# Kernel tuning notes

Measured on AMD Instinct MI355X. Metric: run time of the kernel, lower is better.

Reference implementation:

```python
import jax, jax.numpy as jnp
import numpy as np

L2_REG = 0.02


def setup_inputs() -> dict:
    key = jax.random.key(0)
    k1, k2 = jax.random.split(key)
    n, d = 4096, 1024
    anchors = jax.random.normal(k1, (n, d), dtype=jnp.float32)
    positives = jax.random.normal(k2, (n, d), dtype=jnp.float32)
    return {"anchors": anchors, "positives": positives}


def reference(anchors, positives):
    # Fused equivalent of the per-row masked_select loop:
    # x[i, j] = a_i . (p_j - p_i) = S[i, j] - S[i, i], for j != i
    n = anchors.shape[0]
    S = anchors @ positives.T                     # (n, n)
    x = S - jnp.diag(S)[:, None]                  # subtract anchor-positive sim per row
    offdiag = ~jnp.eye(n, dtype=bool)
    # sum over negatives j != i of exp(x[i, j])
    s = jnp.sum(jnp.where(offdiag, jnp.exp(x), 0.0), axis=1)  # (n,)
    n_pair = jnp.mean(jnp.log1p(s))
    l2 = jnp.sum(anchors ** 2 + positives ** 2) / n
    return n_pair + L2_REG * l2
```

## Files before the change

### kernel.cpp

```cpp
#include <hip/hip_runtime.h>
#include <math.h>
#include <stdint.h>

#define N 4096
#define Dm 1024
#define BK 64
#define NT (Dm / BK)
#define NCB (N / 64)
#define NPART 512

typedef __attribute__((ext_vector_type(8))) short bf16x8;
typedef __attribute__((ext_vector_type(4))) float f32x4;

typedef const void __attribute__((address_space(1)))* gas_t;
typedef void __attribute__((address_space(3)))* las_t;

static __device__ __forceinline__ void gload_lds16(const void* g, void* l) {
    __builtin_amdgcn_global_load_lds((gas_t)g, (las_t)l, 16, 0, 0);
}

static __device__ __forceinline__ unsigned short f2bf(float f) {
    unsigned int u = __float_as_uint(f);
    unsigned int r = (u + 0x7fff + ((u >> 16) & 1)) >> 16;
    return (unsigned short)r;
}

__global__ __launch_bounds__(256) void prep_kernel(const float* __restrict__ A,
                                                   const float* __restrict__ P,
                                                   unsigned short* __restrict__ Abf,
                                                   unsigned short* __restrict__ Pbf,
                                                   float* __restrict__ D,
                                                   float* __restrict__ rowl2) {
    int t = threadIdx.x;
    int lane = t & 63;
    int row = blockIdx.x * 4 + (t >> 6);
    const float4* a4 = (const float4*)(A + (size_t)row * Dm);
    const float4* p4 = (const float4*)(P + (size_t)row * Dm);
    ushort4* ao = (ushort4*)(Abf + (size_t)row * Dm);
    ushort4* po = (ushort4*)(Pbf + (size_t)row * Dm);
    float dot = 0.0f, l2 = 0.0f;
#pragma unroll
    for (int c = 0; c < 4; ++c) {
        int idx = c * 64 + lane;
        float4 a = a4[idx], p = p4[idx];
        ushort4 ab, pb;
        ab.x = f2bf(a.x); ab.y = f2bf(a.y); ab.z = f2bf(a.z); ab.w = f2bf(a.w);
        pb.x = f2bf(p.x); pb.y = f2bf(p.y); pb.z = f2bf(p.z); pb.w = f2bf(p.w);
        ao[idx] = ab; po[idx] = pb;
        dot += a.x * p.x + a.y * p.y + a.z * p.z + a.w * p.w;
        l2  += a.x * a.x + a.y * a.y + a.z * a.z + a.w * a.w
             + p.x * p.x + p.y * p.y + p.z * p.z + p.w * p.w;
    }
#pragma unroll
    for (int off = 32; off; off >>= 1) {
        dot += __shfl_xor(dot, off, 64);
        l2  += __shfl_xor(l2,  off, 64);
    }
    if (lane == 0) {
        D[row]     = dot;
        rowl2[row] = l2;
    }
}

#define STAGE_TILE(gp, lp, kt) do {                                            \
        gload_lds16((gp) + (kt),                    (lp)         + tid * 8);   \
        gload_lds16((gp) + (kt) +  64 * (size_t)Dm, (lp) + 4096  + tid * 8);   \
        gload_lds16((gp) + (kt) + 128 * (size_t)Dm, (lp) + 8192  + tid * 8);   \
        gload_lds16((gp) + (kt) + 192 * (size_t)Dm, (lp) + 12288 + tid * 8);   \
    } while (0)

#define STAGE_B_HALF(lpB, kt, h) do {                                          \
        gload_lds16(gB + (kt) + ((h) ? 128 * (size_t)Dm : (size_t)0),          \
                    (lpB) + (h) * 8192 + tid * 8);                             \
        gload_lds16(gB + (kt) + ((h) ? 192 * (size_t)Dm : 64 * (size_t)Dm),    \
                    (lpB) + (h) * 8192 + 4096 + tid * 8);                      \
    } while (0)

#define READ_A4(dst, buf, rg0) do {                                            \
        dst[0] = *(const bf16x8*)((buf) + ((rg0)     * 16) * BK + aoff0);      \
        dst[1] = *(const bf16x8*)((buf) + ((rg0)     * 16) * BK + aoff1);      \
        dst[2] = *(const bf16x8*)((buf) + ((rg0) + 1) * 16 * BK + aoff0);      \
        dst[3] = *(const bf16x8*)((buf) + ((rg0) + 1) * 16 * BK + aoff1);      \
    } while (0)

#define READ_B8(PAR, buf) do {                                                 \
        _Pragma("unroll")                                                      \
        for (int j = 0; j < 4; ++j) {                                          \
            bfr[PAR][j][0] = *(const bf16x8*)((buf) + j * 16 * BK + aoff0);    \
            bfr[PAR][j][1] = *(const bf16x8*)((buf) + j * 16 * BK + aoff1);    \
        }                                                                      \
    } while (0)

#define MFMA_PH(P, ap, BP)                                                     \
    _Pragma("unroll")                                                          \
    for (int j = 0; j < 4; ++j)                                                \
        acc[2*(P)][j]   = __builtin_amdgcn_mfma_f32_16x16x32_bf16(ap[0], bfr[BP][j][0], acc[2*(P)][j],   0, 0, 0); \
    _Pragma("unroll")                                                          \
    for (int j = 0; j < 4; ++j)                                                \
        acc[2*(P)][j]   = __builtin_amdgcn_mfma_f32_16x16x32_bf16(ap[1], bfr[BP][j][1], acc[2*(P)][j],   0, 0, 0); \
    _Pragma("unroll")                                                          \
    for (int j = 0; j < 4; ++j)                                                \
        acc[2*(P)+1][j] = __builtin_amdgcn_mfma_f32_16x16x32_bf16(ap[2], bfr[BP][j][0], acc[2*(P)+1][j], 0, 0, 0); \
    _Pragma("unroll")                                                          \
    for (int j = 0; j < 4; ++j)                                                \
        acc[2*(P)+1][j] = __builtin_amdgcn_mfma_f32_16x16x32_bf16(ap[3], bfr[BP][j][1], acc[2*(P)+1][j], 0, 0, 0);

#define TILE_BODY(CUR, NXT) do {                                               \
        const unsigned short* aT  = aBase + (CUR) * 16384;                     \
        const unsigned short* aTn = aBase + (NXT) * 16384;                     \
        const unsigned short* bTn = bBase + (NXT) * 16384;                     \
        unsigned short* stA = &As[NXT][0];                                     \
        unsigned short* stB = &Bs[CUR][0];                                     \
         \
        READ_A4(aF[1], aT, 2);                                                 \
        if (t >= 1 && t <= 14) STAGE_TILE(gA, stA, (t + 1) * BK);              \
        __builtin_amdgcn_sched_barrier(0);                                     \
        __builtin_amdgcn_s_setprio(1);                                         \
        MFMA_PH(0, aF[0], CUR)                                                 \
        __builtin_amdgcn_s_setprio(0);                                         \
        __builtin_amdgcn_sched_barrier(0);                                     \
        __builtin_amdgcn_s_barrier();                                          \
         \
        READ_A4(aF[0], aT, 4);                                                 \
        if (t <= 13) STAGE_B_HALF(stB, (t + 2) * BK, 0);                       \
        __builtin_amdgcn_sched_barrier(0);                                     \
        __builtin_amdgcn_s_setprio(1);                                         \
        MFMA_PH(1, aF[1], CUR)                                                 \
        __builtin_amdgcn_s_setprio(0);                                         \
        __builtin_amdgcn_sched_barrier(0);                                     \
        __builtin_amdgcn_s_barrier();                                          \
         \
        READ_A4(aF[1], aT, 6);                                                 \
        if (t <= 13) STAGE_B_HALF(stB, (t + 2) * BK, 1);                       \
        __builtin_amdgcn_sched_barrier(0);                                     \
        __builtin_amdgcn_s_setprio(1);                                         \
        MFMA_PH(2, aF[0], CUR)                                                 \
        __builtin_amdgcn_s_setprio(0);                                         \
        __builtin_amdgcn_sched_barrier(0);                                     \
        __builtin_amdgcn_s_barrier();                                          \
           \
        if (t <= 13)      { asm volatile("s_waitcnt vmcnt(4)" ::: "memory"); } \
        else if (t == 14) { asm volatile("s_waitcnt vmcnt(0)" ::: "memory"); } \
        if (t <= 14) {                                                         \
            __builtin_amdgcn_s_barrier();                                      \
            __builtin_amdgcn_sched_barrier(0);                                 \
            READ_B8(NXT, bTn);                                                 \
            READ_A4(aF[0], aTn, 0);                                            \
        }                                                                      \
        __builtin_amdgcn_sched_barrier(0);                                     \
        __builtin_amdgcn_s_setprio(1);                                         \
        MFMA_PH(3, aF[1], CUR)                                                 \
        __builtin_amdgcn_s_setprio(0);                                         \
        __builtin_amdgcn_sched_barrier(0);                                     \
        if (t <= 13) __builtin_amdgcn_s_barrier();                             \
    } while (0)

__global__ __launch_bounds__(512, 2) void npair_mfma(const unsigned short* __restrict__ Abf,
                                                     const unsigned short* __restrict__ Pbf,
                                                     const float* __restrict__ D,
                                                     float* __restrict__ Mpart,
                                                     float* __restrict__ Spart) {
    __shared__ unsigned short As[2][256 * BK];
    __shared__ unsigned short Bs[2][256 * BK];

    int tid = threadIdx.x;
    int lane = tid & 63;
    int wid = tid >> 6;
    int wr = wid >> 2, wc = wid & 3;

    int bid = blockIdx.y * gridDim.x + blockIdx.x;
    int xcd = bid & 7, lid = bid >> 3;
    int by = (xcd >> 1) * 4 + (lid >> 3);
    int bx = (xcd & 1) * 8 + (lid & 7);
    int row0 = by * 256, col0 = bx * 256;

    int srow = tid >> 3;
    int kcol = (tid & 7) ^ (srow & 7);
    const unsigned short* gA = Abf + (size_t)(row0 + srow) * Dm + (kcol << 3);
    const unsigned short* gB = Pbf + (size_t)(col0 + srow) * Dm + (kcol << 3);

    STAGE_TILE(gA, &As[0][0], 0);
    STAGE_TILE(gB, &Bs[0][0], 0);
    STAGE_TILE(gA, &As[1][0], BK);
    STAGE_TILE(gB, &Bs[1][0], BK);
    asm volatile("s_waitcnt vmcnt(8)" ::: "memory");
    __builtin_amdgcn_s_barrier();
    __builtin_amdgcn_sched_barrier(0);

    int l15 = lane & 15;
    int aoff0 = (((lane >> 4)    ) ^ (lane & 7)) << 3;
    int aoff1 = (((lane >> 4) + 4) ^ (lane & 7)) << 3;
    const unsigned short* aBase = &As[0][0] + (wr * 128 + l15) * BK;
    const unsigned short* bBase = &Bs[0][0] + (wc * 64  + l15) * BK;

    f32x4 acc[8][4] = {};
    bf16x8 bfr[2][4][2];
    bf16x8 aF[2][4];

    READ_B8(0, bBase);
    READ_A4(aF[0], aBase, 0);

    for (int tt = 0; tt < NT / 2; ++tt) {
        int t = 2 * tt;
        TILE_BODY(0, 1);
        t = 2 * tt + 1;
        TILE_BODY(1, 0);
    }

    __builtin_amdgcn_sched_barrier(0);

    int cb = bx * 4 + wc;
#pragma unroll
    for (int i = 0; i < 8; ++i) {
        int rloc = wr * 128 + i * 16 + ((lane >> 4) << 2);
#pragma unroll
        for (int e = 0; e < 4; ++e) {
            int gr = row0 + rloc + e;
            float Dv = D[gr];
            float xs[4];
            float m = -INFINITY;
#pragma unroll
            for (int j = 0; j < 4; ++j) {
                int gc = col0 + wc * 64 + j * 16 + (lane & 15);
                float x = acc[i][j][e] - Dv;
                if (gr == gc) x = -INFINITY;
                xs[j] = x;
                m = fmaxf(m, x);
            }
#pragma unroll
            for (int off = 8; off; off >>= 1) m = fmaxf(m, __shfl_xor(m, off, 64));
            float s = 0.0f;
#pragma unroll
            for (int j = 0; j < 4; ++j) s += __expf(xs[j] - m);
#pragma unroll
            for (int off = 8; off; off >>= 1) s += __shfl_xor(s, off, 64);
            if ((lane & 15) == 0) {
                Mpart[(size_t)gr * NCB + cb] = m;
                Spart[(size_t)gr * NCB + cb] = s;
            }
        }
    }
}

__global__ __launch_bounds__(256) void combine_rows(const float* __restrict__ Mpart,
                                                    const float* __restrict__ Spart,
                                                    const float* __restrict__ rowl2,
                                                    float* __restrict__ partL,
                                                    float* __restrict__ partR) {
    int t = threadIdx.x;
    int lane = t & 63;
    int w = t >> 6;
    __shared__ float ls[8];
#pragma unroll
    for (int r = 0; r < 2; ++r) {
        int row = blockIdx.x * 8 + w * 2 + r;
        float mp = Mpart[(size_t)row * NCB + lane];
        float sp = Spart[(size_t)row * NCB + lane];
        float m = mp;
#pragma unroll
        for (int off = 32; off; off >>= 1) m = fmaxf(m, __shfl_xor(m, off, 64));
        float s = sp * __expf(mp - m);
#pragma unroll
        for (int off = 32; off; off >>= 1) s += __shfl_xor(s, off, 64);
        if (lane == 0) ls[w * 2 + r] = m + logf(__expf(-m) + s);
    }
    __syncthreads();
    if (t == 0) {
        int r8 = blockIdx.x * 8;
        float L = 0.0f, R = 0.0f;
#pragma unroll
        for (int r = 0; r < 8; ++r) { L += ls[r]; R += rowl2[r8 + r]; }
        partL[blockIdx.x] = L;
        partR[blockIdx.x] = R;
    }
}

__global__ __launch_bounds__(256) void final_reduce(const float* __restrict__ partL,
                                                    const float* __restrict__ partR,
                                                    float* __restrict__ out) {
    int t = threadIdx.x;
    float accL = partL[t] + partL[t + 256];
    float acc2 = partR[t] + partR[t + 256];
#pragma unroll
    for (int off = 32; off; off >>= 1) {
        accL += __shfl_xor(accL, off, 64);
        acc2 += __shfl_xor(acc2, off, 64);
    }
    __shared__ float sa[4], sb[4];
    int wave = t >> 6;
    if ((t & 63) == 0) { sa[wave] = accL; sb[wave] = acc2; }
    __syncthreads();
    if (t == 0) {
        float L  = sa[0] + sa[1] + sa[2] + sa[3];
        float l2 = sb[0] + sb[1] + sb[2] + sb[3];
        out[0] = L / (float)N + 0.02f * (l2 / (float)N);
    }
}

extern "C" void kernel_launch(void* const* d_in, const int* in_sizes, int n_in,
                              void* d_out, int out_size, void* d_ws, size_t ws_size,
                              hipStream_t stream) {
    const float* A = (const float*)d_in[0];
    const float* P = (const float*)d_in[1];
    float* out = (float*)d_out;

    unsigned short* Abf = (unsigned short*)d_ws;
    unsigned short* Pbf = Abf + (size_t)N * Dm;
    float* D     = (float*)(Pbf + (size_t)N * Dm);
    float* rowl2 = D + N;
    float* partL = rowl2 + N;
    float* partR = partL + NPART;
    float* Mpart = partR + NPART;
    float* Spart = Mpart + (size_t)N * NCB;

    prep_kernel<<<N / 4, 256, 0, stream>>>(A, P, Abf, Pbf, D, rowl2);
    dim3 grid(16, 16);
    npair_mfma<<<grid, 512, 0, stream>>>(Abf, Pbf, D, Mpart, Spart);
    combine_rows<<<N / 8, 256, 0, stream>>>(Mpart, Spart, rowl2, partL, partR);
    final_reduce<<<1, 256, 0, stream>>>(partL, partR, out);
}
```

Before: 122.3 us.

## Merge final reduce into combine via atomics, move diag subtraction, single-buffer B fragments

Fuses the final reduction into the row-combine kernel using atomic accumulators and a ticket counter, which removes one kernel launch. The diagonal subtraction moves out of the GEMM epilogue into the combine step, applied in log space with a stable softplus. The GEMM main loop drops the double-buffered B register fragments and restructures its phase barriers with explicit LDS waitcnts, which lowers register pressure but removes some load/compute overlap. Float atomics make the summation order nondeterministic.

```diff
diff --git a/kernel.cpp b/kernel.cpp
--- a/kernel.cpp
+++ b/kernel.cpp
@@ -30,7 +30,13 @@
                                                    unsigned short* __restrict__ Abf,
                                                    unsigned short* __restrict__ Pbf,
                                                    float* __restrict__ D,
-                                                   float* __restrict__ rowl2) {
+                                                   float* __restrict__ rowl2,
+                                                   float* __restrict__ accL,
+                                                   float* __restrict__ accR,
+                                                   unsigned int* __restrict__ ticket) {
+    if (blockIdx.x == 0 && threadIdx.x == 0) {
+        accL[0] = 0.0f; accR[0] = 0.0f; ticket[0] = 0u;
+    }
     int t = threadIdx.x;
     int lane = t & 63;
     int row = blockIdx.x * 4 + (t >> 6);
@@ -83,27 +89,34 @@
         dst[3] = *(const bf16x8*)((buf) + ((rg0) + 1) * 16 * BK + aoff1);      \
     } while (0)
 
-#define READ_B8(PAR, buf) do {                                                 \
+#define READ_B8(buf) do {                                                      \
         _Pragma("unroll")                                                      \
         for (int j = 0; j < 4; ++j) {                                          \
-            bfr[PAR][j][0] = *(const bf16x8*)((buf) + j * 16 * BK + aoff0);    \
-            bfr[PAR][j][1] = *(const bf16x8*)((buf) + j * 16 * BK + aoff1);    \
+            bfr[j][0] = *(const bf16x8*)((buf) + j * 16 * BK + aoff0);         \
+            bfr[j][1] = *(const bf16x8*)((buf) + j * 16 * BK + aoff1);         \
         }                                                                      \
     } while (0)
 
-#define MFMA_PH(P, ap, BP)                                                     \
+#define MFMA_PH(P, ap)                                                         \
     _Pragma("unroll")                                                          \
     for (int j = 0; j < 4; ++j)                                                \
-        acc[2*(P)][j]   = __builtin_amdgcn_mfma_f32_16x16x32_bf16(ap[0], bfr[BP][j][0], acc[2*(P)][j],   0, 0, 0); \
+        acc[2*(P)][j]   = __builtin_amdgcn_mfma_f32_16x16x32_bf16(ap[0], bfr[j][0], acc[2*(P)][j],   0, 0, 0); \
     _Pragma("unroll")                                                          \
     for (int j = 0; j < 4; ++j)                                                \
-        acc[2*(P)][j]   = __builtin_amdgcn_mfma_f32_16x16x32_bf16(ap[1], bfr[BP][j][1], acc[2*(P)][j],   0, 0, 0); \
+        acc[2*(P)][j]   = __builtin_amdgcn_mfma_f32_16x16x32_bf16(ap[1], bfr[j][1], acc[2*(P)][j],   0, 0, 0); \
     _Pragma("unroll")                                                          \
     for (int j = 0; j < 4; ++j)                                                \
-        acc[2*(P)+1][j] = __builtin_amdgcn_mfma_f32_16x16x32_bf16(ap[2], bfr[BP][j][0], acc[2*(P)+1][j], 0, 0, 0); \
+        acc[2*(P)+1][j] = __builtin_amdgcn_mfma_f32_16x16x32_bf16(ap[2], bfr[j][0], acc[2*(P)+1][j], 0, 0, 0); \
     _Pragma("unroll")                                                          \
     for (int j = 0; j < 4; ++j)                                                \
-        acc[2*(P)+1][j] = __builtin_amdgcn_mfma_f32_16x16x32_bf16(ap[3], bfr[BP][j][1], acc[2*(P)+1][j], 0, 0, 0);
+        acc[2*(P)+1][j] = __builtin_amdgcn_mfma_f32_16x16x32_bf16(ap[3], bfr[j][1], acc[2*(P)+1][j], 0, 0, 0);
+
+#define PHASE_EDGE() do {                                                      \
+        __builtin_amdgcn_sched_barrier(0);                                     \
+        __builtin_amdgcn_s_barrier();                                          \
+        asm volatile("s_waitcnt lgkmcnt(0)" ::: "memory");                     \
+        __builtin_amdgcn_sched_barrier(0);                                     \
+    } while (0)
 
 #define TILE_BODY(CUR, NXT) do {                                               \
         const unsigned short* aT  = aBase + (CUR) * 16384;                     \
@@ -111,53 +124,44 @@
         const unsigned short* bTn = bBase + (NXT) * 16384;                     \
         unsigned short* stA = &As[NXT][0];                                     \
         unsigned short* stB = &Bs[CUR][0];                                     \
-         \
+           \
         READ_A4(aF[1], aT, 2);                                                 \
         if (t >= 1 && t <= 14) STAGE_TILE(gA, stA, (t + 1) * BK);              \
-        __builtin_amdgcn_sched_barrier(0);                                     \
         __builtin_amdgcn_s_setprio(1);                                         \
-        MFMA_PH(0, aF[0], CUR)                                                 \
+        MFMA_PH(0, aF[0])                                                      \
+        __builtin_amdgcn_s_setprio(0);                                         \
+        PHASE_EDGE();                                                          \
+             \
+        READ_A4(aF[0], aT, 4);                                                 \
+        if (t <= 13) STAGE_B_HALF(stB, (t + 2) * BK, 0);                       \
+        __builtin_amdgcn_s_setprio(1);                                         \
+        MFMA_PH(1, aF[1])                                                      \
+        __builtin_amdgcn_s_setprio(0);                                         \
+        PHASE_EDGE();                                                          \
+             \
+        READ_A4(aF[1], aT, 6);                                                 \
+        if (t <= 13) STAGE_B_HALF(stB, (t + 2) * BK, 1);                       \
+        __builtin_amdgcn_s_setprio(1);                                         \
+        MFMA_PH(2, aF[0])                                                      \
+        __builtin_amdgcn_s_setprio(0);                                         \
+        PHASE_EDGE();                                                          \
+        \
+        __builtin_amdgcn_s_setprio(1);                                         \
+        MFMA_PH(3, aF[1])                                                      \
         __builtin_amdgcn_s_setprio(0);                                         \
         __builtin_amdgcn_sched_barrier(0);                                     \
-        __builtin_amdgcn_s_barrier();                                          \
-         \
-        READ_A4(aF[0], aT, 4);                                                 \
-        if (t <= 13) STAGE_B_HALF(stB, (t + 2) * BK, 0);                       \
-        __builtin_amdgcn_sched_barrier(0);                                     \
-        __builtin_amdgcn_s_setprio(1);                                         \
-        MFMA_PH(1, aF[1], CUR)                                                 \
-        __builtin_amdgcn_s_setprio(0);                                         \
-        __builtin_amdgcn_sched_barrier(0);                                     \
-        __builtin_amdgcn_s_barrier();                                          \
-         \
-        READ_A4(aF[1], aT, 6);                                                 \
-        if (t <= 13) STAGE_B_HALF(stB, (t + 2) * BK, 1);                       \
-        __builtin_amdgcn_sched_barrier(0);                                     \
-        __builtin_amdgcn_s_setprio(1);                                         \
-        MFMA_PH(2, aF[0], CUR)                                                 \
-        __builtin_amdgcn_s_setprio(0);                                         \
-        __builtin_amdgcn_sched_barrier(0);                                     \
-        __builtin_amdgcn_s_barrier();                                          \
-           \
         if (t <= 13)      { asm volatile("s_waitcnt vmcnt(4)" ::: "memory"); } \
         else if (t == 14) { asm volatile("s_waitcnt vmcnt(0)" ::: "memory"); } \
         if (t <= 14) {                                                         \
             __builtin_amdgcn_s_barrier();                                      \
-            __builtin_amdgcn_sched_barrier(0);                                 \
-            READ_B8(NXT, bTn);                                                 \
+            READ_B8(bTn);                                                      \
             READ_A4(aF[0], aTn, 0);                                            \
+            PHASE_EDGE();                                                      \
         }                                                                      \
-        __builtin_amdgcn_sched_barrier(0);                                     \
-        __builtin_amdgcn_s_setprio(1);                                         \
-        MFMA_PH(3, aF[1], CUR)                                                 \
-        __builtin_amdgcn_s_setprio(0);                                         \
-        __builtin_amdgcn_sched_barrier(0);                                     \
-        if (t <= 13) __builtin_amdgcn_s_barrier();                             \
     } while (0)
 
 __global__ __launch_bounds__(512, 2) void npair_mfma(const unsigned short* __restrict__ Abf,
                                                      const unsigned short* __restrict__ Pbf,
-                                                     const float* __restrict__ D,
                                                      float* __restrict__ Mpart,
                                                      float* __restrict__ Spart) {
     __shared__ unsigned short As[2][256 * BK];
@@ -185,7 +189,6 @@
     STAGE_TILE(gB, &Bs[1][0], BK);
     asm volatile("s_waitcnt vmcnt(8)" ::: "memory");
     __builtin_amdgcn_s_barrier();
-    __builtin_amdgcn_sched_barrier(0);
 
     int l15 = lane & 15;
     int aoff0 = (((lane >> 4)    ) ^ (lane & 7)) << 3;
@@ -194,11 +197,14 @@
     const unsigned short* bBase = &Bs[0][0] + (wc * 64  + l15) * BK;
 
     f32x4 acc[8][4] = {};
-    bf16x8 bfr[2][4][2];
+    bf16x8 bfr[4][2];
     bf16x8 aF[2][4];
 
-    READ_B8(0, bBase);
+    READ_B8(bBase);
     READ_A4(aF[0], aBase, 0);
+    __builtin_amdgcn_sched_barrier(0);
+    asm volatile("s_waitcnt lgkmcnt(0)" ::: "memory");
+    __builtin_amdgcn_sched_barrier(0);
 
     for (int tt = 0; tt < NT / 2; ++tt) {
         int t = 2 * tt;
@@ -216,13 +222,12 @@
 #pragma unroll
         for (int e = 0; e < 4; ++e) {
             int gr = row0 + rloc + e;
-            float Dv = D[gr];
             float xs[4];
             float m = -INFINITY;
 #pragma unroll
             for (int j = 0; j < 4; ++j) {
                 int gc = col0 + wc * 64 + j * 16 + (lane & 15);
-                float x = acc[i][j][e] - Dv;
+                float x = acc[i][j][e];
                 if (gr == gc) x = -INFINITY;
                 xs[j] = x;
                 m = fmaxf(m, x);
@@ -242,11 +247,14 @@
     }
 }
 
-__global__ __launch_bounds__(256) void combine_rows(const float* __restrict__ Mpart,
-                                                    const float* __restrict__ Spart,
-                                                    const float* __restrict__ rowl2,
-                                                    float* __restrict__ partL,
-                                                    float* __restrict__ partR) {
+__global__ __launch_bounds__(256) void combine_final(const float* __restrict__ Mpart,
+                                                     const float* __restrict__ Spart,
+                                                     const float* __restrict__ D,
+                                                     const float* __restrict__ rowl2,
+                                                     float* __restrict__ accL,
+                                                     float* __restrict__ accR,
+                                                     unsigned int* __restrict__ ticket,
+                                                     float* __restrict__ out) {
     int t = threadIdx.x;
     int lane = t & 63;
     int w = t >> 6;
@@ -262,7 +270,10 @@
         float s = sp * __expf(mp - m);
 #pragma unroll
         for (int off = 32; off; off >>= 1) s += __shfl_xor(s, off, 64);
-        if (lane == 0) ls[w * 2 + r] = m + logf(__expf(-m) + s);
+        if (lane == 0) {
+            float z = m + logf(s) - D[row];
+            ls[w * 2 + r] = fmaxf(z, 0.0f) + log1pf(__expf(-fabsf(z)));
+        }
     }
     __syncthreads();
     if (t == 0) {
@@ -270,30 +281,15 @@
         float L = 0.0f, R = 0.0f;
 #pragma unroll
         for (int r = 0; r < 8; ++r) { L += ls[r]; R += rowl2[r8 + r]; }
-        partL[blockIdx.x] = L;
-        partR[blockIdx.x] = R;
-    }
-}
-
-__global__ __launch_bounds__(256) void final_reduce(const float* __restrict__ partL,
-                                                    const float* __restrict__ partR,
-                                                    float* __restrict__ out) {
-    int t = threadIdx.x;
-    float accL = partL[t] + partL[t + 256];
-    float acc2 = partR[t] + partR[t + 256];
-#pragma unroll
-    for (int off = 32; off; off >>= 1) {
-        accL += __shfl_xor(accL, off, 64);
-        acc2 += __shfl_xor(acc2, off, 64);
-    }
-    __shared__ float sa[4], sb[4];
-    int wave = t >> 6;
-    if ((t & 63) == 0) { sa[wave] = accL; sb[wave] = acc2; }
-    __syncthreads();
-    if (t == 0) {
-        float L  = sa[0] + sa[1] + sa[2] + sa[3];
-        float l2 = sb[0] + sb[1] + sb[2] + sb[3];
-        out[0] = L / (float)N + 0.02f * (l2 / (float)N);
+        atomicAdd(accL, L);
+        atomicAdd(accR, R);
+        __threadfence();
+        unsigned int done = atomicAdd(ticket, 1u);
+        if (done == NPART - 1) {
+            float aL = atomicAdd(accL, 0.0f);
+            float aR = atomicAdd(accR, 0.0f);
+            out[0] = aL / (float)N + 0.02f * (aR / (float)N);
+        }
     }
 }
 
@@ -308,14 +304,14 @@
     unsigned short* Pbf = Abf + (size_t)N * Dm;
     float* D     = (float*)(Pbf + (size_t)N * Dm);
     float* rowl2 = D + N;
-    float* partL = rowl2 + N;
-    float* partR = partL + NPART;
-    float* Mpart = partR + NPART;
+    float* accL  = rowl2 + N;
+    float* accR  = accL + 1;
+    unsigned int* ticket = (unsigned int*)(accR + 1);
+    float* Mpart = (float*)(ticket + 1);
     float* Spart = Mpart + (size_t)N * NCB;
 
-    prep_kernel<<<N / 4, 256, 0, stream>>>(A, P, Abf, Pbf, D, rowl2);
+    prep_kernel<<<N / 4, 256, 0, stream>>>(A, P, Abf, Pbf, D, rowl2, accL, accR, ticket);
     dim3 grid(16, 16);
-    npair_mfma<<<grid, 512, 0, stream>>>(Abf, Pbf, D, Mpart, Spart);
-    combine_rows<<<N / 8, 256, 0, stream>>>(Mpart, Spart, rowl2, partL, partR);
-    final_reduce<<<1, 256, 0, stream>>>(partL, partR, out);
-}
+    npair_mfma<<<grid, 512, 0, stream>>>(Abf, Pbf, Mpart, Spart);
+    combine_final<<<N / 8, 256, 0, stream>>>(Mpart, Spart, D, rowl2, accL, accR, ticket, out);
+}
```

Result: slower. 136.3 us (+11.5%).
